# Performance work log

Hardware: AMD Instinct MI355X
Metric: run time of the kernel (lower is better)

Reference implementation:

```python
import jax, jax.numpy as jnp
import numpy as np

NEG_INF = -1e30  # stand-in for -inf that is safe under fp16/bf16


def setup_inputs() -> dict:
    key = jax.random.key(0)
    k1, k2, k3, k4, k5 = jax.random.split(key, 5)
    B, NC, H, Wd = 32, 256, 64, 64
    MW, E = 32, 768
    images = jax.random.normal(k1, (B, NC, H, Wd), dtype=jnp.float32)
    words = jax.random.normal(k2, (B, MW, E), dtype=jnp.float32)
    # mask: True where word is ignored; ensure at least one word is attended per row
    mask = jax.random.randint(k3, (B, MW), 0, 2).astype(bool)
    mask = mask.at[:, 0].set(False)
    W = jax.random.normal(k4, (NC, E), dtype=jnp.float32) * (1.0 / np.sqrt(E))
    b = jax.random.normal(k5, (NC,), dtype=jnp.float32) * 0.01
    return {"images": images, "words": words, "mask": mask, "W": W, "b": b}


def reference(images, words, mask, W, b):
    B, NC, H, Wd = images.shape
    _, MW, E = words.shape
    # 1x1 conv over words == linear projection emb_dim -> nc_in
    # words_p: [B, nc_in, max_words]
    words_p = jnp.einsum('bme,ce->bcm', words, W) + b[None, :, None]
    # images flattened to pixels: [B, h*w, nc_in]
    imgs = images.reshape(B, NC, H * Wd).transpose(0, 2, 1)
    # attention scores: [B, h*w, max_words], scaled by 1/sqrt(nc_in)
    attn = jnp.einsum('bpc,bcm->bpm', imgs, words_p) * (1.0 / np.sqrt(NC))
    attn = jnp.where(mask[:, None, :], NEG_INF, attn)
    attn = jax.nn.softmax(attn, axis=-1)
    # weighted word sum per pixel: [B, nc_in, h*w]
    weighted = jnp.einsum('bcm,bpm->bcp', words_p, attn)
    weighted_words = weighted.reshape(B, NC, H, Wd)
    attn_out = attn.transpose(0, 2, 1).reshape(B, MW, H, Wd)
    return weighted_words, attn_out
```

## Files before the change

### kernel.cpp

```cpp
#include <hip/hip_runtime.h>
#include <math.h>

#define B_   32
#define NC_  256
#define HW_  4096
#define MW_  32
#define E_   768
#define NEG_BIG -3.0e38f

typedef float vf2 __attribute__((ext_vector_type(2)));
typedef float vf4 __attribute__((ext_vector_type(4)));

#define PART_OFF   0
#define WT_OFF     2359296
#define WORDST_OFF 2555904

__global__ __launch_bounds__(256) void prep_kernel(
    const float* __restrict__ W, const float* __restrict__ words,
    float* __restrict__ WT, float* __restrict__ wordsT) {
  const int tid = threadIdx.x;
  const int tx = tid & 31, ty = tid >> 5;
  if (blockIdx.x < 192) {
    __shared__ float t[32][33];
    const int tc = blockIdx.x / 24, te = blockIdx.x % 24;
    const int c0 = tc * 32, e0 = te * 32;
#pragma unroll
    for (int k = 0; k < 4; ++k) {
      const int r = ty + 8 * k;
      t[r][tx] = W[(c0 + r) * E_ + e0 + tx];
    }
    __syncthreads();
#pragma unroll
    for (int k = 0; k < 4; ++k) {
      const int r = ty + 8 * k;
      WT[(e0 + r) * NC_ + c0 + tx] = t[tx][r];
    }
  } else {
    __shared__ float t[32][33];
    const int idx = blockIdx.x - 192;
    const int b = idx / 24, te = idx % 24;
    const int e0 = te * 32;
    const float* wsrc = words + (size_t)b * MW_ * E_;
    float* wdst = wordsT + (size_t)b * E_ * MW_;
#pragma unroll
    for (int k = 0; k < 4; ++k) {
      const int m = ty + 8 * k;
      t[m][tx] = wsrc[m * E_ + e0 + tx];
    }
    __syncthreads();
#pragma unroll
    for (int k = 0; k < 4; ++k) {
      const int e = ty + 8 * k;
      wdst[(e0 + e) * MW_ + tx] = t[tx][e];
    }
  }
}

__global__ __launch_bounds__(256) void stage1_partial(
    const float* __restrict__ wordsT, const float* __restrict__ WT,
    float* __restrict__ part) {
  const int c = threadIdx.x;
  const int b = blockIdx.x >> 3;
  const int chunk = blockIdx.x & 7;
  const int e0 = chunk * 96;
  const float* wt = wordsT + (size_t)b * E_ * MW_;
  float acc[32];
#pragma unroll
  for (int m = 0; m < 32; ++m) acc[m] = 0.f;
#pragma unroll 2
  for (int e = e0; e < e0 + 96; ++e) {
    const float wv = WT[(size_t)e * NC_ + c];
    const float* wr = wt + e * MW_;
#pragma unroll
    for (int m = 0; m < 32; ++m) acc[m] = fmaf(wv, wr[m], acc[m]);
  }
  float* pp = part + ((size_t)chunk * 32 + b) * 32 * 256;
#pragma unroll
  for (int m = 0; m < 32; ++m) pp[m * 256 + c] = acc[m];
}

__global__ __launch_bounds__(128, 1) void attention_fused(
    const float* __restrict__ images, const float* __restrict__ part,
    const float* __restrict__ bias, const void* __restrict__ mask_raw,
    float* __restrict__ out_w, float* __restrict__ out_a) {
  __shared__ float lwp[NC_ * MW_];
  __shared__ int is_word;
  const int tid = threadIdx.x;
  const int b = blockIdx.x & 31;
  const int po = ((blockIdx.x >> 5) << 7) + tid;
  const vf4* imgb = (const vf4*)(images + (size_t)b * NC_ * HW_);

  if (tid == 0) is_word = 1;

  vf4 cur[8];
#pragma unroll
  for (int j = 0; j < 8; ++j)
    cur[j] = __builtin_nontemporal_load(&imgb[((size_t)j << 10) + po]);

  {
    vf4* dst = (vf4*)lwp;
#pragma unroll
    for (int k2 = 0; k2 < 16; ++k2) {
      const int v = tid + (k2 << 7);
      const int c = v >> 3;
      const int mq = v & 7;
      const float bc = bias[c];
      float v0 = bc, v1 = bc, v2 = bc, v3 = bc;
#pragma unroll
      for (int pk = 0; pk < 8; ++pk) {
        const float* pp = part + (((size_t)pk * 32 + b) * 32) * 256;
        const int mb = mq << 2;
        v0 += pp[(mb + 0) * 256 + c];
        v1 += pp[(mb + 1) * 256 + c];
        v2 += pp[(mb + 2) * 256 + c];
        v3 += pp[(mb + 3) * 256 + c];
      }
      vf4 t; t.x = v0; t.y = v1; t.z = v2; t.w = v3;
      dst[v] = t;
    }
  }
  __syncthreads();

  {
    const int* mi = (const int*)mask_raw;
#pragma unroll
    for (int q = 0; q < 2; ++q) {
      const int v = mi[q * 128 + tid];
      if (v != 0 && v != 1 && v != 0x3F800000) is_word = 0;
    }
  }
  __syncthreads();
  unsigned mbits = 0;
  if (is_word) {
    const int* mi = (const int*)mask_raw;
#pragma unroll
    for (int m = 0; m < 32; ++m)
      mbits |= (mi[(b << 5) + m] != 0 ? 1u : 0u) << m;
  } else {
    const unsigned char* mb = (const unsigned char*)mask_raw;
#pragma unroll
    for (int m = 0; m < 32; ++m)
      mbits |= (mb[(b << 5) + m] != 0 ? 1u : 0u) << m;
  }

  float s0[32], s1[32], s2[32], s3[32];
#pragma unroll
  for (int m = 0; m < 32; ++m) { s0[m] = 0.f; s1[m] = 0.f; s2[m] = 0.f; s3[m] = 0.f; }

#pragma unroll 1
  for (int c0 = 0; c0 < 256; c0 += 8) {
    vf4 nxt[8];
    if (c0 + 8 < 256) {
#pragma unroll
      for (int j = 0; j < 8; ++j)
        nxt[j] = __builtin_nontemporal_load(&imgb[((size_t)(c0 + 8 + j) << 10) + po]);
    }
#pragma unroll
    for (int j = 0; j < 8; ++j) {
      const float* wr = lwp + ((c0 + j) << 5);
      const vf4 v = cur[j];
#pragma unroll
      for (int m = 0; m < 32; ++m) {
        s0[m] = fmaf(v.x, wr[m], s0[m]);
        s1[m] = fmaf(v.y, wr[m], s1[m]);
        s2[m] = fmaf(v.z, wr[m], s2[m]);
        s3[m] = fmaf(v.w, wr[m], s3[m]);
      }
    }
#pragma unroll
    for (int j = 0; j < 8; ++j) cur[j] = nxt[j];
  }

  float mx0 = NEG_BIG, mx1 = NEG_BIG, mx2 = NEG_BIG, mx3 = NEG_BIG;
#pragma unroll
  for (int m = 0; m < 32; ++m) {
    s0[m] *= 0.0625f; s1[m] *= 0.0625f; s2[m] *= 0.0625f; s3[m] *= 0.0625f;
    if (!((mbits >> m) & 1u)) {
      mx0 = fmaxf(mx0, s0[m]); mx1 = fmaxf(mx1, s1[m]);
      mx2 = fmaxf(mx2, s2[m]); mx3 = fmaxf(mx3, s3[m]);
    }
  }
  float sum0 = 0.f, sum1 = 0.f, sum2 = 0.f, sum3 = 0.f;
#pragma unroll
  for (int m = 0; m < 32; ++m) {
    const bool msk = (mbits >> m) & 1u;
    const float e0 = msk ? 0.f : __expf(s0[m] - mx0);
    const float e1 = msk ? 0.f : __expf(s1[m] - mx1);
    const float e2 = msk ? 0.f : __expf(s2[m] - mx2);
    const float e3 = msk ? 0.f : __expf(s3[m] - mx3);
    s0[m] = e0; s1[m] = e1; s2[m] = e2; s3[m] = e3;
    sum0 += e0; sum1 += e1; sum2 += e2; sum3 += e3;
  }
  const float inv0 = 1.f / sum0, inv1 = 1.f / sum1;
  const float inv2 = 1.f / sum2, inv3 = 1.f / sum3;
  vf4* oa = (vf4*)out_a;
#pragma unroll
  for (int m = 0; m < 32; ++m) {
    s0[m] *= inv0; s1[m] *= inv1; s2[m] *= inv2; s3[m] *= inv3;
    vf4 a; a.x = s0[m]; a.y = s1[m]; a.z = s2[m]; a.w = s3[m];
    __builtin_nontemporal_store(a, &oa[((size_t)((b << 5) + m) << 10) + po]);
  }

  vf4* ow = (vf4*)out_w;
#pragma unroll 1
  for (int c0 = 0; c0 < 256; c0 += 8) {
#pragma unroll
    for (int j = 0; j < 8; ++j) {
      const int c = c0 + j;
      const float* wr = lwp + (c << 5);
      float o0 = 0.f, o1 = 0.f, o2 = 0.f, o3 = 0.f;
#pragma unroll
      for (int m = 0; m < 32; ++m) {
        o0 = fmaf(wr[m], s0[m], o0);
        o1 = fmaf(wr[m], s1[m], o1);
        o2 = fmaf(wr[m], s2[m], o2);
        o3 = fmaf(wr[m], s3[m], o3);
      }
      vf4 o; o.x = o0; o.y = o1; o.z = o2; o.w = o3;
      __builtin_nontemporal_store(o, &ow[((size_t)((b << 8) + c) << 10) + po]);
    }
  }
}

extern "C" void kernel_launch(void* const* d_in, const int* in_sizes, int n_in,
                              void* d_out, int out_size, void* d_ws, size_t ws_size,
                              hipStream_t stream) {
  const float* images = (const float*)d_in[0];
  const float* words  = (const float*)d_in[1];
  const void*  mask   = d_in[2];
  const float* W      = (const float*)d_in[3];
  const float* bias   = (const float*)d_in[4];

  float* ws     = (float*)d_ws;
  float* part   = ws + PART_OFF;
  float* WT     = ws + WT_OFF;
  float* wordsT = ws + WORDST_OFF;

  float* out_w = (float*)d_out;
  float* out_a = out_w + (size_t)B_ * NC_ * HW_;

  prep_kernel<<<960, 256, 0, stream>>>(W, words, WT, wordsT);
  stage1_partial<<<256, 256, 0, stream>>>(wordsT, WT, part);
  attention_fused<<<256, 128, 0, stream>>>(images, part, bias, mask, out_w, out_a);
}
```

Before: 362.2 us.

## Split channel reduction across two half-blocks with LDS exchange of scores

The attention kernel now launches 256 threads per block instead of 128. Each pair of waves handles half of the 256 channels for the same 128 pixel quads. Partial attention scores are summed across the halves through a shared-memory exchange buffer, and then each half computes the softmax redundantly. Each half writes its own half of the weighted-word channels, and only half 0 writes the attention map. The aim is more waves per CU to hide memory latency, since the previous grid had only 256 blocks of 2 waves. The cost is extra LDS traffic, several block barriers, and duplicated softmax work.

```diff
diff --git a/kernel.cpp b/kernel.cpp
--- a/kernel.cpp
+++ b/kernel.cpp
@@ -79,29 +79,35 @@
   for (int m = 0; m < 32; ++m) pp[m * 256 + c] = acc[m];
 }
 
-__global__ __launch_bounds__(128, 1) void attention_fused(
+__global__ __launch_bounds__(256, 1) void attention_fused(
     const float* __restrict__ images, const float* __restrict__ part,
     const float* __restrict__ bias, const void* __restrict__ mask_raw,
     float* __restrict__ out_w, float* __restrict__ out_a) {
   __shared__ float lwp[NC_ * MW_];
+  __shared__ vf4 xbuf[2][8][128];
   __shared__ int is_word;
   const int tid = threadIdx.x;
+  const int lane = tid & 63;
+  const int w = tid >> 6;
+  const int h = w & 1;
+  const int q = lane + ((w >> 1) << 6);
   const int b = blockIdx.x & 31;
-  const int po = ((blockIdx.x >> 5) << 7) + tid;
-  const vf4* imgb = (const vf4*)(images + (size_t)b * NC_ * HW_);
+  const int po = ((blockIdx.x >> 5) << 7) + q;
+  const vf4* imgh = (const vf4*)(images + (size_t)b * NC_ * HW_)
+                    + (((size_t)(h << 7)) << 10) + po;
 
   if (tid == 0) is_word = 1;
 
   vf4 cur[8];
 #pragma unroll
   for (int j = 0; j < 8; ++j)
-    cur[j] = __builtin_nontemporal_load(&imgb[((size_t)j << 10) + po]);
+    cur[j] = __builtin_nontemporal_load(&imgh[(size_t)j << 10]);
 
   {
     vf4* dst = (vf4*)lwp;
 #pragma unroll
-    for (int k2 = 0; k2 < 16; ++k2) {
-      const int v = tid + (k2 << 7);
+    for (int k2 = 0; k2 < 8; ++k2) {
+      const int v = tid + (k2 << 8);
       const int c = v >> 3;
       const int mq = v & 7;
       const float bc = bias[c];
@@ -119,15 +125,11 @@
       dst[v] = t;
     }
   }
-  __syncthreads();
 
   {
     const int* mi = (const int*)mask_raw;
-#pragma unroll
-    for (int q = 0; q < 2; ++q) {
-      const int v = mi[q * 128 + tid];
-      if (v != 0 && v != 1 && v != 0x3F800000) is_word = 0;
-    }
+    const int vv = mi[tid];
+    if (vv != 0 && vv != 1 && vv != 0x3F800000) is_word = 0;
   }
   __syncthreads();
   unsigned mbits = 0;
@@ -148,16 +150,16 @@
   for (int m = 0; m < 32; ++m) { s0[m] = 0.f; s1[m] = 0.f; s2[m] = 0.f; s3[m] = 0.f; }
 
 #pragma unroll 1
-  for (int c0 = 0; c0 < 256; c0 += 8) {
+  for (int c0 = 0; c0 < 128; c0 += 8) {
     vf4 nxt[8];
-    if (c0 + 8 < 256) {
+    if (c0 + 8 < 128) {
 #pragma unroll
       for (int j = 0; j < 8; ++j)
-        nxt[j] = __builtin_nontemporal_load(&imgb[((size_t)(c0 + 8 + j) << 10) + po]);
+        nxt[j] = __builtin_nontemporal_load(&imgh[(size_t)(c0 + 8 + j) << 10]);
     }
 #pragma unroll
     for (int j = 0; j < 8; ++j) {
-      const float* wr = lwp + ((c0 + j) << 5);
+      const float* wr = lwp + (((h << 7) + c0 + j) << 5);
       const vf4 v = cur[j];
 #pragma unroll
       for (int m = 0; m < 32; ++m) {
@@ -170,6 +172,32 @@
 #pragma unroll
     for (int j = 0; j < 8; ++j) cur[j] = nxt[j];
   }
+
+  const int ho = h ^ 1;
+#define XCHG(SV)                                                        \
+  {                                                                     \
+    _Pragma("unroll")                                                   \
+    for (int vq = 0; vq < 8; ++vq) {                                    \
+      vf4 t;                                                            \
+      t.x = SV[4*vq]; t.y = SV[4*vq+1]; t.z = SV[4*vq+2]; t.w = SV[4*vq+3]; \
+      xbuf[h][vq][q] = t;                                               \
+    }                                                                   \
+    __syncthreads();                                                    \
+    _Pragma("unroll")                                                   \
+    for (int vq = 0; vq < 8; ++vq) {                                    \
+      const vf4 t = xbuf[ho][vq][q];                                    \
+      SV[4*vq] += t.x; SV[4*vq+1] += t.y;                               \
+      SV[4*vq+2] += t.z; SV[4*vq+3] += t.w;                             \
+    }                                                                   \
+  }
+  XCHG(s0);
+  __syncthreads();
+  XCHG(s1);
+  __syncthreads();
+  XCHG(s2);
+  __syncthreads();
+  XCHG(s3);
+#undef XCHG
 
   float mx0 = NEG_BIG, mx1 = NEG_BIG, mx2 = NEG_BIG, mx3 = NEG_BIG;
 #pragma unroll
@@ -193,20 +221,25 @@
   }
   const float inv0 = 1.f / sum0, inv1 = 1.f / sum1;
   const float inv2 = 1.f / sum2, inv3 = 1.f / sum3;
-  vf4* oa = (vf4*)out_a;
 #pragma unroll
   for (int m = 0; m < 32; ++m) {
     s0[m] *= inv0; s1[m] *= inv1; s2[m] *= inv2; s3[m] *= inv3;
-    vf4 a; a.x = s0[m]; a.y = s1[m]; a.z = s2[m]; a.w = s3[m];
-    __builtin_nontemporal_store(a, &oa[((size_t)((b << 5) + m) << 10) + po]);
+  }
+  if (h == 0) {
+    vf4* oa = (vf4*)out_a;
+#pragma unroll
+    for (int m = 0; m < 32; ++m) {
+      vf4 a; a.x = s0[m]; a.y = s1[m]; a.z = s2[m]; a.w = s3[m];
+      __builtin_nontemporal_store(a, &oa[(((size_t)(b << 5) + m) << 10) + po]);
+    }
   }
 
   vf4* ow = (vf4*)out_w;
 #pragma unroll 1
-  for (int c0 = 0; c0 < 256; c0 += 8) {
+  for (int c0 = 0; c0 < 128; c0 += 8) {
 #pragma unroll
     for (int j = 0; j < 8; ++j) {
-      const int c = c0 + j;
+      const int c = (h << 7) + c0 + j;
       const float* wr = lwp + (c << 5);
       float o0 = 0.f, o1 = 0.f, o2 = 0.f, o3 = 0.f;
 #pragma unroll
@@ -217,7 +250,7 @@
         o3 = fmaf(wr[m], s3[m], o3);
       }
       vf4 o; o.x = o0; o.y = o1; o.z = o2; o.w = o3;
-      __builtin_nontemporal_store(o, &ow[((size_t)((b << 8) + c) << 10) + po]);
+      __builtin_nontemporal_store(o, &ow[(((size_t)(b << 8) + c) << 10) + po]);
     }
   }
 }
@@ -241,5 +274,5 @@
 
   prep_kernel<<<960, 256, 0, stream>>>(W, words, WT, wordsT);
   stage1_partial<<<256, 256, 0, stream>>>(wordsT, WT, part);
-  attention_fused<<<256, 128, 0, stream>>>(images, part, bias, mask, out_w, out_a);
-}
+  attention_fused<<<256, 256, 0, stream>>>(images, part, bias, mask, out_w, out_a);
+}
```

Measured after the change: 310.5 us. 1.17x faster.
